# Performance work log

Hardware: AMD Instinct MI355X
Metric: run time of the kernel (lower is better)

The kernel has to match this reference:

```python
import jax, jax.numpy as jnp
import numpy as np

HID = 128
MAX_NODES = 100000
MAX_EDGES = 300000
EVT_LEN = 4096
NUM_NODE = 20000
NUM_EDGE = 320000
# EVENT_TYPE_ID_MAP: pad=0 start=1 end=2 node-add=3 node-delete=4 edge-add=5 edge-delete=6
NODE_ADD, NODE_DEL = 3, 4


def time_encode(t, time_w, time_b):
    # TimeEncoder: cos(Linear(1 -> hidden)(t))
    return jnp.cos(t[..., None] * time_w + time_b)


def gru_cell(x, h, w_ih, w_hh, b_ih, b_hh):
    gi = x @ w_ih.T + b_ih
    gh = h @ w_hh.T + b_hh
    i_r, i_z, i_n = jnp.split(gi, 3, axis=-1)
    h_r, h_z, h_n = jnp.split(gh, 3, axis=-1)
    r = jax.nn.sigmoid(i_r + h_r)
    z = jax.nn.sigmoid(i_z + h_z)
    n = jnp.tanh(i_n + r * h_n)
    return (1.0 - z) * n + z * h


def setup_inputs() -> dict:
    key = jax.random.key(0)
    ks = jax.random.split(key, 32)
    H = HID
    s = 0.05
    inp = {}
    inp["event_type_ids"] = jax.random.randint(ks[0], (EVT_LEN,), 0, 7)
    inp["src_ids"] = jax.random.randint(ks[1], (EVT_LEN,), 0, MAX_NODES)
    inp["src_mask"] = (jax.random.uniform(ks[2], (EVT_LEN,)) > 0.3).astype(jnp.float32)
    inp["dst_ids"] = jax.random.randint(ks[3], (EVT_LEN,), 0, MAX_NODES)
    inp["dst_mask"] = (jax.random.uniform(ks[4], (EVT_LEN,)) > 0.3).astype(jnp.float32)
    inp["event_edge_ids"] = jax.random.randint(ks[5], (EVT_LEN,), 0, MAX_EDGES)
    inp["event_embeddings"] = jax.random.normal(ks[6], (EVT_LEN, H), dtype=jnp.float32)
    inp["event_mask"] = (jax.random.uniform(ks[7], (EVT_LEN,)) > 0.2).astype(jnp.float32)
    inp["event_timestamps"] = jax.random.uniform(ks[8], (EVT_LEN,)) * 100.0
    inp["node_ids"] = jax.random.randint(ks[9], (NUM_NODE,), 0, MAX_NODES)
    inp["edge_ids"] = jax.random.randint(ks[10], (NUM_EDGE,), 0, MAX_EDGES)
    inp["edge_index"] = jax.random.randint(ks[11], (2, NUM_EDGE), 0, NUM_NODE)
    inp["time"] = 100
    # persistent-buffer state
    inp["memory"] = jax.random.normal(ks[12], (MAX_NODES, H), dtype=jnp.float32) * s
    inp["last_update"] = jax.random.uniform(ks[13], (MAX_EDGES,)) * 50.0
    inp["node_features"] = jax.random.normal(ks[14], (MAX_NODES, H), dtype=jnp.float32) * s
    inp["edge_features"] = jax.random.normal(ks[15], (MAX_EDGES, H), dtype=jnp.float32) * s
    # TimeEncoder params (Linear(1, H))
    inp["time_w"] = jax.random.normal(ks[16], (H,), dtype=jnp.float32) * s
    inp["time_b"] = jax.random.normal(ks[17], (H,), dtype=jnp.float32) * s
    # GRUCell(5H -> H)
    inp["gru_w_ih"] = jax.random.normal(ks[18], (3 * H, 5 * H), dtype=jnp.float32) * s
    inp["gru_w_hh"] = jax.random.normal(ks[19], (3 * H, H), dtype=jnp.float32) * s
    inp["gru_b_ih"] = jax.random.normal(ks[20], (3 * H,), dtype=jnp.float32) * s
    inp["gru_b_hh"] = jax.random.normal(ks[21], (3 * H,), dtype=jnp.float32) * s
    # TransformerConv(H, H, heads=1, edge_dim=2H)
    inp["wq"] = jax.random.normal(ks[22], (H, H), dtype=jnp.float32) * s
    inp["bq"] = jax.random.normal(ks[23], (H,), dtype=jnp.float32) * s
    inp["wk"] = jax.random.normal(ks[24], (H, H), dtype=jnp.float32) * s
    inp["bk"] = jax.random.normal(ks[25], (H,), dtype=jnp.float32) * s
    inp["wv"] = jax.random.normal(ks[26], (H, H), dtype=jnp.float32) * s
    inp["bv"] = jax.random.normal(ks[27], (H,), dtype=jnp.float32) * s
    inp["we"] = jax.random.normal(ks[28], (H, 2 * H), dtype=jnp.float32) * s  # lin_edge, no bias
    inp["wskip"] = jax.random.normal(ks[29], (H, H), dtype=jnp.float32) * s
    inp["bskip"] = jax.random.normal(ks[30], (H,), dtype=jnp.float32) * s
    return inp


def reference(event_type_ids, src_ids, src_mask, dst_ids, dst_mask, event_edge_ids,
              event_embeddings, event_mask, event_timestamps, node_ids, edge_ids,
              edge_index, time, memory, last_update, node_features, edge_features,
              time_w, time_b, gru_w_ih, gru_w_hh, gru_b_ih, gru_b_hh,
              wq, bq, wk, bk, wv, bv, we, wskip, bskip):
    H = HID
    # ---- message() ----
    L = event_type_ids.shape[0]
    type_embs = jnp.broadcast_to(event_type_ids[:, None].astype(memory.dtype), (L, H))
    src_embs = memory[src_ids] * src_mask[:, None]
    dst_embs = memory[dst_ids] * dst_mask[:, None]
    edge_last = last_update[event_edge_ids]
    rel_ts = event_timestamps - edge_last * dst_mask
    is_node_ev = ((event_type_ids == NODE_ADD) | (event_type_ids == NODE_DEL)).astype(event_timestamps.dtype)
    ts_emb = time_encode(event_timestamps * is_node_ev + rel_ts * dst_mask, time_w, time_b) * event_mask[:, None]
    src_msgs = jnp.concatenate([type_embs, src_embs, dst_embs, ts_emb, event_embeddings], axis=1) * event_mask[:, None]
    dst_msgs = jnp.concatenate([type_embs, dst_embs, src_embs, ts_emb, event_embeddings], axis=1) * dst_mask[:, None]
    # ---- agg_message(): scatter-mean over node ids ----
    def agg(msgs, ids):
        s = jax.ops.segment_sum(msgs, ids, num_segments=MAX_NODES)
        c = jax.ops.segment_sum(jnp.ones((msgs.shape[0],), msgs.dtype), ids, num_segments=MAX_NODES)
        return s / jnp.maximum(c, 1.0)[:, None]
    agg_src = agg(src_msgs, src_ids)
    agg_dst = agg(dst_msgs, dst_ids)
    # ---- GRU memory update on unique ids ----
    # torch: memory[cat(uniq_src, uniq_dst)] = rnn(...); reads use pre-update memory,
    # dst writes come after src writes so they override on overlap. Duplicate ids in
    # src_ids carry identical per-id values, so scatter-set is equivalent to unique().
    new_src = gru_cell(agg_src[src_ids], memory[src_ids], gru_w_ih, gru_w_hh, gru_b_ih, gru_b_hh)
    new_dst = gru_cell(agg_dst[dst_ids], memory[dst_ids], gru_w_ih, gru_w_hh, gru_b_ih, gru_b_hh)
    memory = memory.at[src_ids].set(new_src)
    memory = memory.at[dst_ids].set(new_dst)
    # ---- edge attributes ----
    rel_t = time - last_update[edge_ids]
    rel_t_embs = time_encode(rel_t, time_w, time_b)
    edge_attr = jnp.concatenate([rel_t_embs, edge_features[edge_ids]], axis=-1)  # (E, 2H)
    # ---- TransformerConv (heads=1, concat, root_weight) ----
    x = node_features[node_ids] + memory[node_ids]  # (N, H)
    src, dst = edge_index[0], edge_index[1]
    q = x @ wq.T + bq
    k = x @ wk.T + bk
    v = x @ wv.T + bv
    e = edge_attr @ we.T  # lin_edge (no bias)
    alpha = jnp.sum(q[dst] * (k[src] + e), axis=-1) / jnp.sqrt(jnp.asarray(H, x.dtype))
    amax = jax.ops.segment_max(alpha, dst, num_segments=x.shape[0])
    ex = jnp.exp(alpha - amax[dst])
    denom = jax.ops.segment_sum(ex, dst, num_segments=x.shape[0])
    p = ex / jnp.maximum(denom[dst], 1e-16)
    out = jax.ops.segment_sum(p[:, None] * (v[src] + e), dst, num_segments=x.shape[0])
    return out + x @ wskip.T + bskip
```

## Files before the change

kernel.cpp:

```cpp
#include <hip/hip_runtime.h>
#include <math.h>

#define HID   128
#define MAXN  100000
#define MAXE  300000
#define EVT   4096
#define NNODE 20000
#define NEDGE 320000

typedef unsigned short u16;
typedef __attribute__((ext_vector_type(8))) short bf16x8;
typedef __attribute__((ext_vector_type(4))) float f32x4;

#define OFF_WIHB      0u
#define OFF_WHHB      491520u
#define OFF_WEB       589824u
#define OFF_WALLB     655360u
#define OFF_BALL      851968u
#define BASE2         855040u
#define OFF_REP_SRC   (BASE2 + 0u)
#define OFF_REP_DST   (BASE2 + 400128u)
#define OFF_CNT_SRC   (BASE2 + 800256u)
#define OFF_CNT_DST   (BASE2 + 1200384u)
#define OFF_SUM_SRC   (BASE2 + 1600512u)
#define OFF_SUM_DST   (BASE2 + 12086272u)
#define OFF_XGB       (BASE2 + 22572032u)
#define OFF_HG        (BASE2 + 33057792u)
#define OFF_HGB       (BASE2 + 37252096u)
#define OFF_GI        (BASE2 + 39349248u)
#define OFF_GH        (BASE2 + 51932160u)
#define OFF_XB        (BASE2 + 0u)
#define OFF_QKVSE     (BASE2 + 5120000u)
#define OFF_KVB       (BASE2 + 66560000u)
#define OFF_DEG       (BASE2 + 76800000u)
#define OFF_OFFS      (BASE2 + 76880128u)
#define OFF_CURSOR    (BASE2 + 76960256u)
#define OFF_SORTED    (BASE2 + 77041664u)
#define OFF_SACCB     (BASE2 + 78321664u)

__device__ __forceinline__ float sigmoidf_(float x) { return 1.f / (1.f + __expf(-x)); }
__device__ __forceinline__ u16 f2b(float f) {
    unsigned u = __float_as_uint(f);
    unsigned r = (u + 0x7fffu + ((u >> 16) & 1u)) >> 16;
    return (u16)r;
}
__device__ __forceinline__ float b2f(unsigned h) { return __uint_as_float(h << 16); }

__global__ void k_prep(const float* __restrict__ w_ih, const float* __restrict__ w_hh,
                       const float* __restrict__ we,
                       const float* __restrict__ wq, const float* __restrict__ wk_,
                       const float* __restrict__ wv, const float* __restrict__ wskip,
                       const float* __restrict__ bq, const float* __restrict__ bk,
                       const float* __restrict__ bv, const float* __restrict__ bskip,
                       u16* __restrict__ w_ih_b, u16* __restrict__ w_hh_b,
                       u16* __restrict__ we_b, u16* __restrict__ Wallb,
                       float* __restrict__ ball, int* __restrict__ deg,
                       char* __restrict__ zbase) {
    int b = blockIdx.x, t = threadIdx.x;
    if (b < 960) {
        int i = b * 256 + t;
        w_ih_b[i] = f2b(w_ih[i]);
        return;
    }
    b -= 960;
    if (b < 192) {
        int i = b * 256 + t;
        w_hh_b[i] = f2b(w_hh[i]);
        return;
    }
    b -= 192;
    if (b < 128) {
        int i = b * 256 + t;
        we_b[i] = f2b(we[i]);
        return;
    }
    b -= 128;
    if (b < 79) {
        int i = b * 256 + t;
        if (i < NNODE) deg[i] = 0;
        return;
    }
    b -= 79;
    if (b < 384) {
        int idx = b * 256 + t;
        int row = idx >> 7;
        int k = idx & 127;
        float v;
        if (row < 128)      v = wq[row * 128 + k];
        else if (row < 256) v = wk_[(row - 128) * 128 + k];
        else if (row < 384) v = wv[(row - 256) * 128 + k];
        else if (row < 512) v = wskip[(row - 384) * 128 + k];
        else {
            int j = row - 512;
            float a = 0.f;
            for (int t2 = 0; t2 < 128; t2++) a += wq[t2 * 128 + k] * we[t2 * 256 + j];
            v = a;
        }
        Wallb[row * 128 + k] = f2b(v);
        if (k == 0) {
            float bb;
            if (row < 128)      bb = bq[row];
            else if (row < 256) bb = bk[row - 128];
            else if (row < 384) bb = bv[row - 256];
            else if (row < 512) bb = bskip[row - 384];
            else { int j = row - 512; float a = 0.f; for (int t2 = 0; t2 < 128; t2++) a += bq[t2] * we[t2 * 256 + j]; bb = a; }
            ball[row] = bb;
        }
        return;
    }
    b -= 384;
    const int NFF = 50016;
    const int NZ  = 1360736;
    uint4 ff = make_uint4(0xFFFFFFFFu, 0xFFFFFFFFu, 0xFFFFFFFFu, 0xFFFFFFFFu);
    uint4 zz = make_uint4(0u, 0u, 0u, 0u);
    int idx = b * 256 + t;
    int stride = 1024 * 256;
    uint4* pff = (uint4*)zbase;
    uint4* pzz = (uint4*)(zbase + 800256);
    for (int i = idx; i < NFF; i += stride) pff[i] = ff;
    for (int i = idx; i < NZ; i += stride) pzz[i] = zz;
}

__global__ void k_tables_deg(const int* __restrict__ src_ids, const int* __restrict__ dst_ids,
                             unsigned* rep_src, unsigned* rep_dst, int* cnt_src, int* cnt_dst,
                             const int* __restrict__ eidx, int* __restrict__ deg) {
    int b = blockIdx.x, t = threadIdx.x;
    if (b < 16) {
        int i = b * 256 + t;
        if (i >= EVT) return;
        int s = src_ids[i], d = dst_ids[i];
        atomicMin(&rep_src[s], (unsigned)i);
        atomicAdd(&cnt_src[s], 1);
        atomicMin(&rep_dst[d], (unsigned)i);
        atomicAdd(&cnt_dst[d], 1);
    } else {
        int j = (b - 16) * 256 + t;
        if (j >= NEDGE) return;
        atomicAdd(&deg[eidx[NEDGE + j]], 1);
    }
}

__global__ void k_message(const int* __restrict__ et_ids, const int* __restrict__ src_ids,
                          const float* __restrict__ src_mask, const int* __restrict__ dst_ids,
                          const float* __restrict__ dst_mask, const int* __restrict__ ev_eids,
                          const float* __restrict__ ev_emb, const float* __restrict__ ev_mask,
                          const float* __restrict__ ev_ts, const float* __restrict__ memory,
                          const float* __restrict__ last_update, const float* __restrict__ time_w,
                          const float* __restrict__ time_b, const unsigned* __restrict__ rep_src,
                          const unsigned* __restrict__ rep_dst, const int* __restrict__ cnt_src,
                          const int* __restrict__ cnt_dst, float* sum_src, float* sum_dst,
                          u16* __restrict__ Xgb, float* __restrict__ Hg, u16* __restrict__ Hgb) {
    int i = blockIdx.x;
    int c = threadIdx.x;
    int et = et_ids[i];
    float sm = src_mask[i], dm = dst_mask[i], em = ev_mask[i], ts = ev_ts[i];
    int sid = src_ids[i], did = dst_ids[i], eid = ev_eids[i];
    float isnode = (et == 3 || et == 4) ? 1.f : 0.f;
    float rel = ts - last_update[eid] * dm;
    float tval = ts * isnode + rel * dm;
    float tse = __cosf(tval * time_w[c] + time_b[c]) * em;
    float typ = (float)et;
    float sv_raw = memory[(size_t)sid * HID + c];
    float dv_raw = memory[(size_t)did * HID + c];
    float sv = sv_raw * sm;
    float dv = dv_raw * dm;
    float ev = ev_emb[(size_t)i * HID + c];
    Hg[(size_t)i * HID + c] = sv_raw;
    Hgb[(size_t)i * HID + c] = f2b(sv_raw);
    Hg[(size_t)(EVT + i) * HID + c] = dv_raw;
    Hgb[(size_t)(EVT + i) * HID + c] = f2b(dv_raw);
    float s0 = typ * em, s1 = sv * em, s2 = dv * em, s3 = tse * em, s4 = ev * em;
    u16* xs = Xgb + (size_t)i * 640;
    xs[c] = f2b(s0); xs[128 + c] = f2b(s1); xs[256 + c] = f2b(s2);
    xs[384 + c] = f2b(s3); xs[512 + c] = f2b(s4);
    if (cnt_src[sid] > 1) {
        float* ps = sum_src + (size_t)rep_src[sid] * 640;
        atomicAdd(ps + c, s0);
        atomicAdd(ps + 128 + c, s1);
        atomicAdd(ps + 256 + c, s2);
        atomicAdd(ps + 384 + c, s3);
        atomicAdd(ps + 512 + c, s4);
    }
    float d0 = typ * dm, d1 = dv * dm, d2 = sv * dm, d3 = tse * dm, d4 = ev * dm;
    u16* xd = Xgb + (size_t)(EVT + i) * 640;
    xd[c] = f2b(d0); xd[128 + c] = f2b(d1); xd[256 + c] = f2b(d2);
    xd[384 + c] = f2b(d3); xd[512 + c] = f2b(d4);
    if (cnt_dst[did] > 1) {
        float* pd = sum_dst + (size_t)rep_dst[did] * 640;
        atomicAdd(pd + c, d0);
        atomicAdd(pd + 128 + c, d1);
        atomicAdd(pd + 256 + c, d2);
        atomicAdd(pd + 384 + c, d3);
        atomicAdd(pd + 512 + c, d4);
    }
}

__global__ void k_fix(const int* __restrict__ src_ids, const int* __restrict__ dst_ids,
                      const unsigned* __restrict__ rep_src, const unsigned* __restrict__ rep_dst,
                      const int* __restrict__ cnt_src, const int* __restrict__ cnt_dst,
                      const float* __restrict__ sum_src, const float* __restrict__ sum_dst,
                      u16* __restrict__ Xgb) {
    int r = blockIdx.x, c = threadIdx.x;
    const float* sum;
    int cnt;
    if (r < EVT) {
        int id = src_ids[r];
        cnt = cnt_src[id];
        if (cnt < 2) return;
        sum = sum_src + (size_t)rep_src[id] * 640;
    } else {
        int id = dst_ids[r - EVT];
        cnt = cnt_dst[id];
        if (cnt < 2) return;
        sum = sum_dst + (size_t)rep_dst[id] * 640;
    }
    float inv = 1.f / (float)cnt;
    u16* x = Xgb + (size_t)r * 640;
#pragma unroll
    for (int y = 0; y < 5; ++y)
        x[y * 128 + c] = f2b(sum[y * 128 + c] * inv);
}

__device__ __forceinline__ void gemm_tile(const u16* __restrict__ A, const u16* __restrict__ W,
                                          const float* __restrict__ bias, float* __restrict__ C,
                                          u16* __restrict__ KVb, int M, int N, int K, int acc,
                                          u16* Als, u16* Wls) {
    int tid = threadIdx.x;
    int bm = blockIdx.x * 128, bn = blockIdx.y * 128;
    int wave = tid >> 6, lane = tid & 63;
    int wm = (wave & 1) * 64, wn = (wave >> 1) * 64;
    int l15 = lane & 15, quad = lane >> 4;
    f32x4 accf[4][4] = {};
    for (int k0 = 0; k0 < K; k0 += 32) {
#pragma unroll
        for (int h = 0; h < 2; ++h) {
            int ch = tid + h * 256;
            int row = ch >> 2, kc = (ch & 3) * 8;
            int gr = bm + row;
            float4 av = make_float4(0.f, 0.f, 0.f, 0.f);
            if (gr < M) av = *(const float4*)(A + (size_t)gr * K + k0 + kc);
            *(float4*)&Als[row * 40 + kc] = av;
            int wr = bn + row;
            float4 wv_ = *(const float4*)(W + (size_t)wr * K + k0 + kc);
            *(float4*)&Wls[row * 40 + kc] = wv_;
        }
        __syncthreads();
        bf16x8 af[4], bfr[4];
#pragma unroll
        for (int r = 0; r < 4; ++r)
            af[r] = *(const bf16x8*)&Als[(wm + r * 16 + l15) * 40 + quad * 8];
#pragma unroll
        for (int c2 = 0; c2 < 4; ++c2)
            bfr[c2] = *(const bf16x8*)&Wls[(wn + c2 * 16 + l15) * 40 + quad * 8];
#pragma unroll
        for (int r = 0; r < 4; ++r)
#pragma unroll
            for (int c2 = 0; c2 < 4; ++c2)
                accf[r][c2] = __builtin_amdgcn_mfma_f32_16x16x32_bf16(af[r], bfr[c2], accf[r][c2], 0, 0, 0);
        __syncthreads();
    }
#pragma unroll
    for (int r = 0; r < 4; ++r) {
#pragma unroll
        for (int c2 = 0; c2 < 4; ++c2) {
            int ncol = bn + wn + c2 * 16 + l15;
            float bv = bias ? bias[ncol] : 0.f;
#pragma unroll
            for (int reg = 0; reg < 4; ++reg) {
                int mrow = bm + wm + r * 16 + quad * 4 + reg;
                if (mrow >= M) continue;
                float v = accf[r][c2][reg] + bv;
                if (KVb && ncol >= 128 && ncol < 384) {
                    KVb[(size_t)mrow * 256 + (ncol - 128)] = f2b(v);
                } else {
                    if (acc) v += C[(size_t)mrow * N + ncol];
                    C[(size_t)mrow * N + ncol] = v;
                }
            }
        }
    }
}

__global__ __launch_bounds__(256) void k_gemm_mfma(const u16* __restrict__ A,
                                                   const u16* __restrict__ W,
                                                   const float* __restrict__ bias,
                                                   float* __restrict__ C,
                                                   u16* __restrict__ KVb,
                                                   int M, int N, int K, int acc) {
    __shared__ u16 Als[128 * 40];
    __shared__ u16 Wls[128 * 40];
    gemm_tile(A, W, bias, C, KVb, M, N, K, acc, Als, Wls);
}

__global__ __launch_bounds__(256) void k_gemm_dual(const u16* __restrict__ A0, const u16* __restrict__ W0,
                                                   const float* __restrict__ b0, float* __restrict__ C0,
                                                   const u16* __restrict__ A1, const u16* __restrict__ W1,
                                                   const float* __restrict__ b1, float* __restrict__ C1) {
    __shared__ u16 Als[128 * 40];
    __shared__ u16 Wls[128 * 40];
    if (blockIdx.z == 0) gemm_tile(A0, W0, b0, C0, nullptr, 2 * EVT, 384, 640, 0, Als, Wls);
    else                 gemm_tile(A1, W1, b1, C1, nullptr, 2 * EVT, 384, 128, 0, Als, Wls);
}

__global__ void k_gru_scatter(const float* __restrict__ Gi, const float* __restrict__ Gh,
                              const float* __restrict__ Hg, const int* __restrict__ src_ids,
                              const int* __restrict__ dst_ids, const unsigned* __restrict__ rep_dst,
                              float* __restrict__ memory) {
    int r = blockIdx.x, c = threadIdx.x;
    const float* gi = Gi + (size_t)r * 384;
    const float* gh = Gh + (size_t)r * 384;
    float rg = sigmoidf_(gi[c] + gh[c]);
    float z  = sigmoidf_(gi[128 + c] + gh[128 + c]);
    float n  = tanhf(gi[256 + c] + rg * gh[256 + c]);
    float h0 = Hg[(size_t)r * HID + c];
    float h  = (1.f - z) * n + z * h0;
    if (r < EVT) {
        int sid = src_ids[r];
        if (rep_dst[sid] == 0xFFFFFFFFu) memory[(size_t)sid * HID + c] = h;
    } else {
        int did = dst_ids[r - EVT];
        memory[(size_t)did * HID + c] = h;
    }
}

__global__ void k_x(const int* __restrict__ node_ids, const float* __restrict__ nf,
                    const float* __restrict__ memory, u16* __restrict__ Xb) {
    int p = blockIdx.x, c = threadIdx.x;
    int nid = node_ids[p];
    Xb[(size_t)p * HID + c] = f2b(nf[(size_t)nid * HID + c] + memory[(size_t)nid * HID + c]);
}

__global__ __launch_bounds__(1024) void k_scan_one(const int* __restrict__ deg,
                                                   int* __restrict__ offs, int* __restrict__ cursor) {
    __shared__ int wsum[16];
    int t = threadIdx.x, lane = t & 63, w = t >> 6;
    int carry = 0;
    const int N4 = NNODE / 4;
    for (int base = 0; base < N4; base += 1024) {
        int i4 = base + t;
        int4 v = make_int4(0, 0, 0, 0);
        if (i4 < N4) v = ((const int4*)deg)[i4];
        int s = v.x + v.y + v.z + v.w;
        int x = s;
#pragma unroll
        for (int d = 1; d < 64; d <<= 1) { int y = __shfl_up(x, d, 64); if (lane >= d) x += y; }
        if (lane == 63) wsum[w] = x;
        __syncthreads();
        int add = 0, tot = 0;
        for (int k2 = 0; k2 < 16; ++k2) { int ss = wsum[k2]; if (k2 < w) add += ss; tot += ss; }
        if (i4 < N4) {
            int e = carry + add + x - s;
            int4 o;
            o.x = e;
            o.y = e + v.x;
            o.z = o.y + v.y;
            o.w = o.z + v.z;
            ((int4*)offs)[i4] = o;
            ((int4*)cursor)[i4] = o;
        }
        carry += tot;
        __syncthreads();
    }
    if (t == 0) offs[NNODE] = NEDGE;
}

__global__ void k_sortscat(const int* __restrict__ eidx, int* __restrict__ cursor,
                           int* __restrict__ sorted) {
    int j = blockIdx.x * blockDim.x + threadIdx.x;
    if (j >= NEDGE) return;
    int d = eidx[NEDGE + j];
    int pos = atomicAdd(&cursor[d], 1);
    sorted[pos] = j;
}

__global__ __launch_bounds__(256) void k_node(const float* __restrict__ QK,
        const u16* __restrict__ KVb, const int* __restrict__ offs,
        const int* __restrict__ sorted, const int* __restrict__ eidx,
        const int* __restrict__ edge_ids, const float* __restrict__ last_update,
        const float* __restrict__ time_w, const float* __restrict__ time_b,
        const float* __restrict__ ef, const int* __restrict__ tptr,
        float* __restrict__ out, u16* __restrict__ saccb) {
    int wave = threadIdx.x >> 6, lane = threadIdx.x & 63;
    int n = blockIdx.x * 4 + wave;
    int c = 2 * lane;
    const float* base = QK + (size_t)n * 768;
    float2 qd   = *(const float2*)(base + c);
    float2 skip = *(const float2*)(base + 384 + c);
    float2 qet  = *(const float2*)(base + 512 + c);
    float2 qef  = *(const float2*)(base + 640 + c);
    float2 tw   = *(const float2*)(time_w + c);
    float2 tb   = *(const float2*)(time_b + c);
    float tf = (float)(*tptr);
    int start = offs[n], end = offs[n + 1];
    int deg = end - start;
    if (deg == 0) {
        *(float2*)(out + (size_t)n * HID + c) = skip;
        *(unsigned*)(saccb + (size_t)n * 256 + c) = 0u;
        *(unsigned*)(saccb + (size_t)n * 256 + 128 + c) = 0u;
        return;
    }
    float m = -1e30f, l_ = 0.f;
    float va0 = 0.f, va1 = 0.f, s00 = 0.f, s01 = 0.f, s10 = 0.f, s11 = 0.f;
    for (int cb = start; cb < end; cb += 64) {
        int cnt = end - cb; if (cnt > 64) cnt = 64;
        int s_l = 0, eid_l = 0; float rt_l = 0.f;
        if (lane < cnt) {
            int j = sorted[cb + lane];
            s_l = eidx[j];
            eid_l = edge_ids[j];
            rt_l = tf - last_update[eid_l];
        }
        for (int e0 = 0; e0 < cnt; e0 += 4) {
            float pv[4], cv0[4], cv1[4], vx[4], vy[4], ex[4], ey[4];
#pragma unroll
            for (int i = 0; i < 4; ++i) {
                int idx = e0 + i;
                int sel = (idx < cnt) ? idx : e0;
                int s   = __shfl(s_l, sel, 64);
                int eid = __shfl(eid_l, sel, 64);
                float rt = __shfl(rt_l, sel, 64);
                unsigned kvp = *(const unsigned*)(KVb + (size_t)s * 256 + c);
                unsigned vvp = *(const unsigned*)(KVb + (size_t)s * 256 + 128 + c);
                float2 ev = *(const float2*)(ef + (size_t)eid * HID + c);
                float k0f = b2f(kvp & 0xffffu), k1f = b2f(kvp >> 16);
                vx[i] = b2f(vvp & 0xffffu); vy[i] = b2f(vvp >> 16);
                cv0[i] = __cosf(rt * tw.x + tb.x);
                cv1[i] = __cosf(rt * tw.y + tb.y);
                ex[i] = ev.x; ey[i] = ev.y;
                pv[i] = qd.x * k0f + qd.y * k1f + qet.x * cv0[i] + qet.y * cv1[i]
                      + qef.x * ev.x + qef.y * ev.y;
            }
#pragma unroll
            for (int msk = 32; msk > 0; msk >>= 1) {
#pragma unroll
                for (int i = 0; i < 4; ++i) pv[i] += __shfl_xor(pv[i], msk, 64);
            }
            float al[4];
#pragma unroll
            for (int i = 0; i < 4; ++i)
                al[i] = (e0 + i < cnt) ? pv[i] * 0.08838834764831845f : -1e30f;
            float gm = fmaxf(fmaxf(al[0], al[1]), fmaxf(al[2], al[3]));
            if (gm > m) {
                float fac = __expf(m - gm);
                l_ *= fac; va0 *= fac; va1 *= fac;
                s00 *= fac; s01 *= fac; s10 *= fac; s11 *= fac;
                m = gm;
            }
#pragma unroll
            for (int i = 0; i < 4; ++i) {
                float w = __expf(al[i] - m);
                l_ += w;
                va0 += w * vx[i]; va1 += w * vy[i];
                s00 += w * cv0[i]; s01 += w * cv1[i];
                s10 += w * ex[i]; s11 += w * ey[i];
            }
        }
    }
    float inv = 1.f / fmaxf(l_, 1e-16f);
    float2 o; o.x = va0 * inv + skip.x; o.y = va1 * inv + skip.y;
    *(float2*)(out + (size_t)n * HID + c) = o;
    unsigned p0 = (unsigned)f2b(s00 * inv) | ((unsigned)f2b(s01 * inv) << 16);
    unsigned p1 = (unsigned)f2b(s10 * inv) | ((unsigned)f2b(s11 * inv) << 16);
    *(unsigned*)(saccb + (size_t)n * 256 + c) = p0;
    *(unsigned*)(saccb + (size_t)n * 256 + 128 + c) = p1;
}

extern "C" void kernel_launch(void* const* d_in, const int* in_sizes, int n_in,
                              void* d_out, int out_size, void* d_ws, size_t ws_size,
                              hipStream_t stream) {
    const int*   et_ids        = (const int*)d_in[0];
    const int*   src_ids       = (const int*)d_in[1];
    const float* src_mask      = (const float*)d_in[2];
    const int*   dst_ids       = (const int*)d_in[3];
    const float* dst_mask      = (const float*)d_in[4];
    const int*   ev_eids       = (const int*)d_in[5];
    const float* ev_emb        = (const float*)d_in[6];
    const float* ev_mask       = (const float*)d_in[7];
    const float* ev_ts         = (const float*)d_in[8];
    const int*   node_ids      = (const int*)d_in[9];
    const int*   edge_ids      = (const int*)d_in[10];
    const int*   edge_index    = (const int*)d_in[11];
    const int*   tptr          = (const int*)d_in[12];
    float*       memory        = (float*)d_in[13];
    const float* last_update   = (const float*)d_in[14];
    const float* node_features = (const float*)d_in[15];
    const float* edge_features = (const float*)d_in[16];
    const float* time_w        = (const float*)d_in[17];
    const float* time_b        = (const float*)d_in[18];
    const float* w_ih          = (const float*)d_in[19];
    const float* w_hh          = (const float*)d_in[20];
    const float* b_ih          = (const float*)d_in[21];
    const float* b_hh          = (const float*)d_in[22];
    const float* wq            = (const float*)d_in[23];
    const float* bq            = (const float*)d_in[24];
    const float* wk            = (const float*)d_in[25];
    const float* bk            = (const float*)d_in[26];
    const float* wv            = (const float*)d_in[27];
    const float* bv            = (const float*)d_in[28];
    const float* we            = (const float*)d_in[29];
    const float* wskip         = (const float*)d_in[30];
    const float* bskip         = (const float*)d_in[31];
    float* out = (float*)d_out;
    char*  wsb = (char*)d_ws;

    u16*   w_ih_b  = (u16*)(wsb + OFF_WIHB);
    u16*   w_hh_b  = (u16*)(wsb + OFF_WHHB);
    u16*   we_b    = (u16*)(wsb + OFF_WEB);
    u16*   Wallb   = (u16*)(wsb + OFF_WALLB);
    float* ball    = (float*)(wsb + OFF_BALL);
    unsigned* rep_src = (unsigned*)(wsb + OFF_REP_SRC);
    unsigned* rep_dst = (unsigned*)(wsb + OFF_REP_DST);
    int*   cnt_src = (int*)(wsb + OFF_CNT_SRC);
    int*   cnt_dst = (int*)(wsb + OFF_CNT_DST);
    float* sum_src = (float*)(wsb + OFF_SUM_SRC);
    float* sum_dst = (float*)(wsb + OFF_SUM_DST);
    u16*   Xgb     = (u16*)(wsb + OFF_XGB);
    float* Hg      = (float*)(wsb + OFF_HG);
    u16*   Hgb     = (u16*)(wsb + OFF_HGB);
    float* Gi      = (float*)(wsb + OFF_GI);
    float* Gh      = (float*)(wsb + OFF_GH);
    u16*   Xb      = (u16*)(wsb + OFF_XB);
    float* QKVSE   = (float*)(wsb + OFF_QKVSE);
    u16*   KVb     = (u16*)(wsb + OFF_KVB);
    int*   deg     = (int*)(wsb + OFF_DEG);
    int*   offs    = (int*)(wsb + OFF_OFFS);
    int*   cursor  = (int*)(wsb + OFF_CURSOR);
    int*   sorted  = (int*)(wsb + OFF_SORTED);
    u16*   saccb   = (u16*)(wsb + OFF_SACCB);

    k_prep<<<2767, 256, 0, stream>>>(w_ih, w_hh, we, wq, wk, wv, wskip, bq, bk, bv, bskip,
                                     w_ih_b, w_hh_b, we_b, Wallb, ball, deg, wsb + OFF_REP_SRC);
    k_tables_deg<<<1266, 256, 0, stream>>>(src_ids, dst_ids, rep_src, rep_dst, cnt_src, cnt_dst,
                                           edge_index, deg);
    k_message<<<EVT, 128, 0, stream>>>(et_ids, src_ids, src_mask, dst_ids, dst_mask, ev_eids,
                                       ev_emb, ev_mask, ev_ts, memory, last_update, time_w, time_b,
                                       rep_src, rep_dst, cnt_src, cnt_dst, sum_src, sum_dst,
                                       Xgb, Hg, Hgb);
    k_fix<<<2 * EVT, 128, 0, stream>>>(src_ids, dst_ids, rep_src, rep_dst,
                                       cnt_src, cnt_dst, sum_src, sum_dst, Xgb);
    k_gemm_dual<<<dim3(64, 3, 2), 256, 0, stream>>>(Xgb, w_ih_b, b_ih, Gi,
                                                    Hgb, w_hh_b, b_hh, Gh);
    k_gru_scatter<<<2 * EVT, 128, 0, stream>>>(Gi, Gh, Hg, src_ids, dst_ids, rep_dst, memory);

    k_x<<<NNODE, 128, 0, stream>>>(node_ids, node_features, memory, Xb);
    k_gemm_mfma<<<dim3(157, 6), 256, 0, stream>>>(Xb, Wallb, ball, QKVSE, KVb, NNODE, 768, 128, 0);
    k_scan_one<<<1, 1024, 0, stream>>>(deg, offs, cursor);
    k_sortscat<<<1250, 256, 0, stream>>>(edge_index, cursor, sorted);
    k_node<<<NNODE / 4, 256, 0, stream>>>(QKVSE, KVb, offs, sorted, edge_index, edge_ids,
                                          last_update, time_w, time_b, edge_features, tptr,
                                          out, saccb);
    k_gemm_mfma<<<dim3(157, 1), 256, 0, stream>>>(saccb, we_b, nullptr, out, nullptr, NNODE, 128, 256, 1);
}
```

Measured before the change: 510.0 us.

## Replace atomic-sum dedup with per-id linked chains and merge small kernels

Duplicate src/dst ids are now tracked with head/chain linked lists built via atomicExch, and k_fix recomputes the mean message by walking each chain, instead of float atomicAdd into large per-id sum buffers. This removes the big zero-fill of those sum buffers and the atomic traffic in the message kernel. Several small launches are also merged: tables/degree counting into the message kernel, the x gather into the scan kernel, and the edge sort-scatter into the QKV GEMM as an extra grid row. The cost is redundant recomputation along chains in k_fix and some load imbalance from the merged launches.

```diff
diff --git a/kernel.cpp b/kernel.cpp
--- a/kernel.cpp
+++ b/kernel.cpp
@@ -18,25 +18,29 @@
 #define OFF_WALLB     655360u
 #define OFF_BALL      851968u
 #define BASE2         855040u
-#define OFF_REP_SRC   (BASE2 + 0u)
-#define OFF_REP_DST   (BASE2 + 400128u)
+#define OFF_HEAD_SRC  (BASE2 + 0u)
+#define OFF_HEAD_DST  (BASE2 + 400128u)
 #define OFF_CNT_SRC   (BASE2 + 800256u)
 #define OFF_CNT_DST   (BASE2 + 1200384u)
-#define OFF_SUM_SRC   (BASE2 + 1600512u)
-#define OFF_SUM_DST   (BASE2 + 12086272u)
+#define OFF_CHAIN_SRC (BASE2 + 1600512u)
+#define OFF_CHAIN_DST (BASE2 + 1616896u)
 #define OFF_XGB       (BASE2 + 22572032u)
 #define OFF_HG        (BASE2 + 33057792u)
 #define OFF_HGB       (BASE2 + 37252096u)
 #define OFF_GI        (BASE2 + 39349248u)
 #define OFF_GH        (BASE2 + 51932160u)
-#define OFF_XB        (BASE2 + 0u)
-#define OFF_QKVSE     (BASE2 + 5120000u)
-#define OFF_KVB       (BASE2 + 66560000u)
-#define OFF_DEG       (BASE2 + 76800000u)
-#define OFF_OFFS      (BASE2 + 76880128u)
-#define OFF_CURSOR    (BASE2 + 76960256u)
-#define OFF_SORTED    (BASE2 + 77041664u)
-#define OFF_SACCB     (BASE2 + 78321664u)
+#define OFF_XB        (BASE2 + 1703936u)
+#define OFF_QKVSE     (BASE2 + 7000064u)
+#undef OFF_XB
+#undef OFF_QKVSE
+#define OFF_XB        (BASE2 + 1703936u)
+#define OFF_QKVSE     (BASE2 + 6823936u)
+#define OFF_KVB       (BASE2 + 68263936u)
+#define OFF_DEG       (BASE2 + 78503936u)
+#define OFF_OFFS      (BASE2 + 78584064u)
+#define OFF_CURSOR    (BASE2 + 78664192u)
+#define OFF_SORTED    (BASE2 + 78744320u)
+#define OFF_SACCB     (BASE2 + 80024320u)
 
 __device__ __forceinline__ float sigmoidf_(float x) { return 1.f / (1.f + __expf(-x)); }
 __device__ __forceinline__ u16 f2b(float f) {
@@ -110,48 +114,46 @@
     }
     b -= 384;
     const int NFF = 50016;
-    const int NZ  = 1360736;
     uint4 ff = make_uint4(0xFFFFFFFFu, 0xFFFFFFFFu, 0xFFFFFFFFu, 0xFFFFFFFFu);
     uint4 zz = make_uint4(0u, 0u, 0u, 0u);
     int idx = b * 256 + t;
-    int stride = 1024 * 256;
+    int stride = 257 * 256;
     uint4* pff = (uint4*)zbase;
     uint4* pzz = (uint4*)(zbase + 800256);
     for (int i = idx; i < NFF; i += stride) pff[i] = ff;
-    for (int i = idx; i < NZ; i += stride) pzz[i] = zz;
-}
-
-__global__ void k_tables_deg(const int* __restrict__ src_ids, const int* __restrict__ dst_ids,
-                             unsigned* rep_src, unsigned* rep_dst, int* cnt_src, int* cnt_dst,
-                             const int* __restrict__ eidx, int* __restrict__ deg) {
-    int b = blockIdx.x, t = threadIdx.x;
-    if (b < 16) {
-        int i = b * 256 + t;
-        if (i >= EVT) return;
-        int s = src_ids[i], d = dst_ids[i];
-        atomicMin(&rep_src[s], (unsigned)i);
-        atomicAdd(&cnt_src[s], 1);
-        atomicMin(&rep_dst[d], (unsigned)i);
-        atomicAdd(&cnt_dst[d], 1);
-    } else {
-        int j = (b - 16) * 256 + t;
-        if (j >= NEDGE) return;
-        atomicAdd(&deg[eidx[NEDGE + j]], 1);
-    }
-}
-
-__global__ void k_message(const int* __restrict__ et_ids, const int* __restrict__ src_ids,
+    for (int i = idx; i < NFF; i += stride) pzz[i] = zz;
+}
+
+__global__ void k_msg_tables(const int* __restrict__ et_ids, const int* __restrict__ src_ids,
                           const float* __restrict__ src_mask, const int* __restrict__ dst_ids,
                           const float* __restrict__ dst_mask, const int* __restrict__ ev_eids,
                           const float* __restrict__ ev_emb, const float* __restrict__ ev_mask,
                           const float* __restrict__ ev_ts, const float* __restrict__ memory,
                           const float* __restrict__ last_update, const float* __restrict__ time_w,
-                          const float* __restrict__ time_b, const unsigned* __restrict__ rep_src,
-                          const unsigned* __restrict__ rep_dst, const int* __restrict__ cnt_src,
-                          const int* __restrict__ cnt_dst, float* sum_src, float* sum_dst,
+                          const float* __restrict__ time_b,
+                          int* __restrict__ head_src, int* __restrict__ head_dst,
+                          int* __restrict__ cnt_src, int* __restrict__ cnt_dst,
+                          int* __restrict__ chain_src, int* __restrict__ chain_dst,
+                          const int* __restrict__ eidx, int* __restrict__ deg,
                           u16* __restrict__ Xgb, float* __restrict__ Hg, u16* __restrict__ Hgb) {
-    int i = blockIdx.x;
-    int c = threadIdx.x;
+    int b = blockIdx.x, t = threadIdx.x;
+    if (b >= EVT) {
+        int bb = b - EVT;
+        if (bb < 32) {
+            int i = bb * 128 + t;
+            int s = src_ids[i], d = dst_ids[i];
+            chain_src[i] = atomicExch(&head_src[s], i);
+            atomicAdd(&cnt_src[s], 1);
+            chain_dst[i] = atomicExch(&head_dst[d], i);
+            atomicAdd(&cnt_dst[d], 1);
+        } else {
+            int j = (bb - 32) * 128 + t;
+            atomicAdd(&deg[eidx[NEDGE + j]], 1);
+        }
+        return;
+    }
+    int i = b;
+    int c = t;
     int et = et_ids[i];
     float sm = src_mask[i], dm = dst_mask[i], em = ev_mask[i], ts = ev_ts[i];
     int sid = src_ids[i], did = dst_ids[i], eid = ev_eids[i];
@@ -169,56 +171,63 @@
     Hgb[(size_t)i * HID + c] = f2b(sv_raw);
     Hg[(size_t)(EVT + i) * HID + c] = dv_raw;
     Hgb[(size_t)(EVT + i) * HID + c] = f2b(dv_raw);
-    float s0 = typ * em, s1 = sv * em, s2 = dv * em, s3 = tse * em, s4 = ev * em;
     u16* xs = Xgb + (size_t)i * 640;
-    xs[c] = f2b(s0); xs[128 + c] = f2b(s1); xs[256 + c] = f2b(s2);
-    xs[384 + c] = f2b(s3); xs[512 + c] = f2b(s4);
-    if (cnt_src[sid] > 1) {
-        float* ps = sum_src + (size_t)rep_src[sid] * 640;
-        atomicAdd(ps + c, s0);
-        atomicAdd(ps + 128 + c, s1);
-        atomicAdd(ps + 256 + c, s2);
-        atomicAdd(ps + 384 + c, s3);
-        atomicAdd(ps + 512 + c, s4);
-    }
-    float d0 = typ * dm, d1 = dv * dm, d2 = sv * dm, d3 = tse * dm, d4 = ev * dm;
+    xs[c] = f2b(typ * em); xs[128 + c] = f2b(sv * em); xs[256 + c] = f2b(dv * em);
+    xs[384 + c] = f2b(tse * em); xs[512 + c] = f2b(ev * em);
     u16* xd = Xgb + (size_t)(EVT + i) * 640;
-    xd[c] = f2b(d0); xd[128 + c] = f2b(d1); xd[256 + c] = f2b(d2);
-    xd[384 + c] = f2b(d3); xd[512 + c] = f2b(d4);
-    if (cnt_dst[did] > 1) {
-        float* pd = sum_dst + (size_t)rep_dst[did] * 640;
-        atomicAdd(pd + c, d0);
-        atomicAdd(pd + 128 + c, d1);
-        atomicAdd(pd + 256 + c, d2);
-        atomicAdd(pd + 384 + c, d3);
-        atomicAdd(pd + 512 + c, d4);
-    }
+    xd[c] = f2b(typ * dm); xd[128 + c] = f2b(dv * dm); xd[256 + c] = f2b(sv * dm);
+    xd[384 + c] = f2b(tse * dm); xd[512 + c] = f2b(ev * dm);
 }
 
 __global__ void k_fix(const int* __restrict__ src_ids, const int* __restrict__ dst_ids,
-                      const unsigned* __restrict__ rep_src, const unsigned* __restrict__ rep_dst,
+                      const int* __restrict__ head_src, const int* __restrict__ head_dst,
+                      const int* __restrict__ chain_src, const int* __restrict__ chain_dst,
                       const int* __restrict__ cnt_src, const int* __restrict__ cnt_dst,
-                      const float* __restrict__ sum_src, const float* __restrict__ sum_dst,
-                      u16* __restrict__ Xgb) {
+                      const int* __restrict__ et_ids, const float* __restrict__ src_mask,
+                      const float* __restrict__ dst_mask, const int* __restrict__ ev_eids,
+                      const float* __restrict__ ev_emb, const float* __restrict__ ev_mask,
+                      const float* __restrict__ ev_ts, const float* __restrict__ memory,
+                      const float* __restrict__ last_update, const float* __restrict__ time_w,
+                      const float* __restrict__ time_b, u16* __restrict__ Xgb) {
     int r = blockIdx.x, c = threadIdx.x;
-    const float* sum;
-    int cnt;
-    if (r < EVT) {
-        int id = src_ids[r];
-        cnt = cnt_src[id];
-        if (cnt < 2) return;
-        sum = sum_src + (size_t)rep_src[id] * 640;
-    } else {
-        int id = dst_ids[r - EVT];
-        cnt = cnt_dst[id];
-        if (cnt < 2) return;
-        sum = sum_dst + (size_t)rep_dst[id] * 640;
+    bool is_src = (r < EVT);
+    int id = is_src ? src_ids[r] : dst_ids[r - EVT];
+    int cnt = is_src ? cnt_src[id] : cnt_dst[id];
+    if (cnt < 2) return;
+    float own = memory[(size_t)id * HID + c];
+    float tw = time_w[c], tb = time_b[c];
+    float a0 = 0.f, a1 = 0.f, a2 = 0.f, a3 = 0.f, a4 = 0.f;
+    int j = is_src ? head_src[id] : head_dst[id];
+    for (int k = 0; k < cnt; ++k) {
+        int et = et_ids[j];
+        float sm = src_mask[j], dm = dst_mask[j], em = ev_mask[j], ts = ev_ts[j];
+        int eid = ev_eids[j];
+        float isnode = (et == 3 || et == 4) ? 1.f : 0.f;
+        float rel = ts - last_update[eid] * dm;
+        float tval = ts * isnode + rel * dm;
+        float tse = __cosf(tval * tw + tb);
+        float ev = ev_emb[(size_t)j * HID + c];
+        float typ = (float)et;
+        if (is_src) {
+            float sv = own * sm;
+            float dv = memory[(size_t)dst_ids[j] * HID + c] * dm;
+            float tsm = tse * em;
+            a0 += typ * em; a1 += sv * em; a2 += dv * em;
+            a3 += tsm * em; a4 += ev * em;
+            j = chain_src[j];
+        } else {
+            float dv = own * dm;
+            float sv = memory[(size_t)src_ids[j] * HID + c] * sm;
+            float tsm = tse * em;
+            a0 += typ * dm; a1 += dv * dm; a2 += sv * dm;
+            a3 += tsm * dm; a4 += ev * dm;
+            j = chain_dst[j];
+        }
     }
     float inv = 1.f / (float)cnt;
     u16* x = Xgb + (size_t)r * 640;
-#pragma unroll
-    for (int y = 0; y < 5; ++y)
-        x[y * 128 + c] = f2b(sum[y * 128 + c] * inv);
+    x[c] = f2b(a0 * inv); x[128 + c] = f2b(a1 * inv); x[256 + c] = f2b(a2 * inv);
+    x[384 + c] = f2b(a3 * inv); x[512 + c] = f2b(a4 * inv);
 }
 
 __device__ __forceinline__ void gemm_tile(const u16* __restrict__ A, const u16* __restrict__ W,
@@ -292,6 +301,28 @@
     gemm_tile(A, W, bias, C, KVb, M, N, K, acc, Als, Wls);
 }
 
+__global__ __launch_bounds__(256) void k_gemm_qkvse(const u16* __restrict__ A,
+                                                    const u16* __restrict__ W,
+                                                    const float* __restrict__ bias,
+                                                    float* __restrict__ C,
+                                                    u16* __restrict__ KVb,
+                                                    const int* __restrict__ eidx,
+                                                    int* __restrict__ cursor,
+                                                    int* __restrict__ sorted) {
+    __shared__ u16 Als[128 * 40];
+    __shared__ u16 Wls[128 * 40];
+    if (blockIdx.y == 6) {
+        int j = blockIdx.x * 256 + threadIdx.x;
+        for (; j < NEDGE; j += 157 * 256) {
+            int d = eidx[NEDGE + j];
+            int pos = atomicAdd(&cursor[d], 1);
+            sorted[pos] = j;
+        }
+        return;
+    }
+    gemm_tile(A, W, bias, C, KVb, NNODE, 768, 128, 0, Als, Wls);
+}
+
 __global__ __launch_bounds__(256) void k_gemm_dual(const u16* __restrict__ A0, const u16* __restrict__ W0,
                                                    const float* __restrict__ b0, float* __restrict__ C0,
                                                    const u16* __restrict__ A1, const u16* __restrict__ W1,
@@ -304,7 +335,7 @@
 
 __global__ void k_gru_scatter(const float* __restrict__ Gi, const float* __restrict__ Gh,
                               const float* __restrict__ Hg, const int* __restrict__ src_ids,
-                              const int* __restrict__ dst_ids, const unsigned* __restrict__ rep_dst,
+                              const int* __restrict__ dst_ids, const int* __restrict__ cnt_dst,
                               float* __restrict__ memory) {
     int r = blockIdx.x, c = threadIdx.x;
     const float* gi = Gi + (size_t)r * 384;
@@ -316,24 +347,29 @@
     float h  = (1.f - z) * n + z * h0;
     if (r < EVT) {
         int sid = src_ids[r];
-        if (rep_dst[sid] == 0xFFFFFFFFu) memory[(size_t)sid * HID + c] = h;
+        if (cnt_dst[sid] == 0) memory[(size_t)sid * HID + c] = h;
     } else {
         int did = dst_ids[r - EVT];
         memory[(size_t)did * HID + c] = h;
     }
 }
 
-__global__ void k_x(const int* __restrict__ node_ids, const float* __restrict__ nf,
-                    const float* __restrict__ memory, u16* __restrict__ Xb) {
-    int p = blockIdx.x, c = threadIdx.x;
-    int nid = node_ids[p];
-    Xb[(size_t)p * HID + c] = f2b(nf[(size_t)nid * HID + c] + memory[(size_t)nid * HID + c]);
-}
-
-__global__ __launch_bounds__(1024) void k_scan_one(const int* __restrict__ deg,
-                                                   int* __restrict__ offs, int* __restrict__ cursor) {
+__global__ __launch_bounds__(1024) void k_x_scan(const int* __restrict__ node_ids,
+                                                 const float* __restrict__ nf,
+                                                 const float* __restrict__ memory,
+                                                 u16* __restrict__ Xb,
+                                                 const int* __restrict__ deg,
+                                                 int* __restrict__ offs,
+                                                 int* __restrict__ cursor) {
     __shared__ int wsum[16];
-    int t = threadIdx.x, lane = t & 63, w = t >> 6;
+    int p = blockIdx.x, t = threadIdx.x;
+    if (p < 2500) {
+        int row = p * 8 + (t >> 7), c = t & 127;
+        int nid = node_ids[row];
+        Xb[(size_t)row * HID + c] = f2b(nf[(size_t)nid * HID + c] + memory[(size_t)nid * HID + c]);
+        return;
+    }
+    int lane = t & 63, w = t >> 6;
     int carry = 0;
     const int N4 = NNODE / 4;
     for (int base = 0; base < N4; base += 1024) {
@@ -362,15 +398,6 @@
         __syncthreads();
     }
     if (t == 0) offs[NNODE] = NEDGE;
-}
-
-__global__ void k_sortscat(const int* __restrict__ eidx, int* __restrict__ cursor,
-                           int* __restrict__ sorted) {
-    int j = blockIdx.x * blockDim.x + threadIdx.x;
-    if (j >= NEDGE) return;
-    int d = eidx[NEDGE + j];
-    int pos = atomicAdd(&cursor[d], 1);
-    sorted[pos] = j;
 }
 
 __global__ __launch_bounds__(256) void k_node(const float* __restrict__ QK,
@@ -503,49 +530,47 @@
     float* out = (float*)d_out;
     char*  wsb = (char*)d_ws;
 
-    u16*   w_ih_b  = (u16*)(wsb + OFF_WIHB);
-    u16*   w_hh_b  = (u16*)(wsb + OFF_WHHB);
-    u16*   we_b    = (u16*)(wsb + OFF_WEB);
-    u16*   Wallb   = (u16*)(wsb + OFF_WALLB);
-    float* ball    = (float*)(wsb + OFF_BALL);
-    unsigned* rep_src = (unsigned*)(wsb + OFF_REP_SRC);
-    unsigned* rep_dst = (unsigned*)(wsb + OFF_REP_DST);
-    int*   cnt_src = (int*)(wsb + OFF_CNT_SRC);
-    int*   cnt_dst = (int*)(wsb + OFF_CNT_DST);
-    float* sum_src = (float*)(wsb + OFF_SUM_SRC);
-    float* sum_dst = (float*)(wsb + OFF_SUM_DST);
-    u16*   Xgb     = (u16*)(wsb + OFF_XGB);
-    float* Hg      = (float*)(wsb + OFF_HG);
-    u16*   Hgb     = (u16*)(wsb + OFF_HGB);
-    float* Gi      = (float*)(wsb + OFF_GI);
-    float* Gh      = (float*)(wsb + OFF_GH);
-    u16*   Xb      = (u16*)(wsb + OFF_XB);
-    float* QKVSE   = (float*)(wsb + OFF_QKVSE);
-    u16*   KVb     = (u16*)(wsb + OFF_KVB);
-    int*   deg     = (int*)(wsb + OFF_DEG);
-    int*   offs    = (int*)(wsb + OFF_OFFS);
-    int*   cursor  = (int*)(wsb + OFF_CURSOR);
-    int*   sorted  = (int*)(wsb + OFF_SORTED);
-    u16*   saccb   = (u16*)(wsb + OFF_SACCB);
-
-    k_prep<<<2767, 256, 0, stream>>>(w_ih, w_hh, we, wq, wk, wv, wskip, bq, bk, bv, bskip,
-                                     w_ih_b, w_hh_b, we_b, Wallb, ball, deg, wsb + OFF_REP_SRC);
-    k_tables_deg<<<1266, 256, 0, stream>>>(src_ids, dst_ids, rep_src, rep_dst, cnt_src, cnt_dst,
-                                           edge_index, deg);
-    k_message<<<EVT, 128, 0, stream>>>(et_ids, src_ids, src_mask, dst_ids, dst_mask, ev_eids,
+    u16*   w_ih_b   = (u16*)(wsb + OFF_WIHB);
+    u16*   w_hh_b   = (u16*)(wsb + OFF_WHHB);
+    u16*   we_b     = (u16*)(wsb + OFF_WEB);
+    u16*   Wallb    = (u16*)(wsb + OFF_WALLB);
+    float* ball     = (float*)(wsb + OFF_BALL);
+    int*   head_src = (int*)(wsb + OFF_HEAD_SRC);
+    int*   head_dst = (int*)(wsb + OFF_HEAD_DST);
+    int*   cnt_src  = (int*)(wsb + OFF_CNT_SRC);
+    int*   cnt_dst  = (int*)(wsb + OFF_CNT_DST);
+    int*   chain_src= (int*)(wsb + OFF_CHAIN_SRC);
+    int*   chain_dst= (int*)(wsb + OFF_CHAIN_DST);
+    u16*   Xgb      = (u16*)(wsb + OFF_XGB);
+    float* Hg       = (float*)(wsb + OFF_HG);
+    u16*   Hgb      = (u16*)(wsb + OFF_HGB);
+    float* Gi       = (float*)(wsb + OFF_GI);
+    float* Gh       = (float*)(wsb + OFF_GH);
+    u16*   Xb       = (u16*)(wsb + OFF_XB);
+    float* QKVSE    = (float*)(wsb + OFF_QKVSE);
+    u16*   KVb      = (u16*)(wsb + OFF_KVB);
+    int*   deg      = (int*)(wsb + OFF_DEG);
+    int*   offs     = (int*)(wsb + OFF_OFFS);
+    int*   cursor   = (int*)(wsb + OFF_CURSOR);
+    int*   sorted   = (int*)(wsb + OFF_SORTED);
+    u16*   saccb    = (u16*)(wsb + OFF_SACCB);
+
+    k_prep<<<2000, 256, 0, stream>>>(w_ih, w_hh, we, wq, wk, wv, wskip, bq, bk, bv, bskip,
+                                     w_ih_b, w_hh_b, we_b, Wallb, ball, deg, wsb + OFF_HEAD_SRC);
+    k_msg_tables<<<6628, 128, 0, stream>>>(et_ids, src_ids, src_mask, dst_ids, dst_mask, ev_eids,
+                                           ev_emb, ev_mask, ev_ts, memory, last_update, time_w, time_b,
+                                           head_src, head_dst, cnt_src, cnt_dst, chain_src, chain_dst,
+                                           edge_index, deg, Xgb, Hg, Hgb);
+    k_fix<<<2 * EVT, 128, 0, stream>>>(src_ids, dst_ids, head_src, head_dst, chain_src, chain_dst,
+                                       cnt_src, cnt_dst, et_ids, src_mask, dst_mask, ev_eids,
                                        ev_emb, ev_mask, ev_ts, memory, last_update, time_w, time_b,
-                                       rep_src, rep_dst, cnt_src, cnt_dst, sum_src, sum_dst,
-                                       Xgb, Hg, Hgb);
-    k_fix<<<2 * EVT, 128, 0, stream>>>(src_ids, dst_ids, rep_src, rep_dst,
-                                       cnt_src, cnt_dst, sum_src, sum_dst, Xgb);
+                                       Xgb);
     k_gemm_dual<<<dim3(64, 3, 2), 256, 0, stream>>>(Xgb, w_ih_b, b_ih, Gi,
                                                     Hgb, w_hh_b, b_hh, Gh);
-    k_gru_scatter<<<2 * EVT, 128, 0, stream>>>(Gi, Gh, Hg, src_ids, dst_ids, rep_dst, memory);
-
-    k_x<<<NNODE, 128, 0, stream>>>(node_ids, node_features, memory, Xb);
-    k_gemm_mfma<<<dim3(157, 6), 256, 0, stream>>>(Xb, Wallb, ball, QKVSE, KVb, NNODE, 768, 128, 0);
-    k_scan_one<<<1, 1024, 0, stream>>>(deg, offs, cursor);
-    k_sortscat<<<1250, 256, 0, stream>>>(edge_index, cursor, sorted);
+    k_gru_scatter<<<2 * EVT, 128, 0, stream>>>(Gi, Gh, Hg, src_ids, dst_ids, cnt_dst, memory);
+    k_x_scan<<<2501, 1024, 0, stream>>>(node_ids, node_features, memory, Xb, deg, offs, cursor);
+    k_gemm_qkvse<<<dim3(157, 7), 256, 0, stream>>>(Xb, Wallb, ball, QKVSE, KVb,
+                                                   edge_index, cursor, sorted);
     k_node<<<NNODE / 4, 256, 0, stream>>>(QKVSE, KVb, offs, sorted, edge_index, edge_ids,
                                           last_update, time_w, time_b, edge_features, tptr,
                                           out, saccb);
```

Measured after the change: 490.1 us. 1.04x faster.
